# Kernel tuning notes

Hardware: AMD Instinct MI355X
Metric: run time of the kernel (lower is better)

The kernel has to match this reference:

```python
import jax, jax.numpy as jnp
import numpy as np

V, E, H, C_TAGS, B, T = 32000, 256, 200, 20, 64, 512
LN_EPS = 1e-5


def setup_inputs() -> dict:
    key = jax.random.key(0)
    ks = jax.random.split(key, 12)
    s = 0.05
    return {
        "words": jax.random.randint(ks[0], (B, T), 0, V),
        "seq_len": jax.random.randint(ks[1], (B,), T // 2, T + 1),
        "target": jax.random.randint(ks[2], (B, T), 0, C_TAGS),
        "embed_table": jax.random.normal(ks[3], (V, E)) * s,
        "ln_gamma": jnp.ones((E,)),
        "ln_beta": jnp.zeros((E,)),
        "w_ih_f": jax.random.normal(ks[4], (4 * H, E)) * s,
        "w_hh_f": jax.random.normal(ks[5], (4 * H, H)) * s,
        "b_f": jnp.zeros((4 * H,)),  # b_ih + b_hh folded together
        "w_ih_b": jax.random.normal(ks[6], (4 * H, E)) * s,
        "w_hh_b": jax.random.normal(ks[7], (4 * H, H)) * s,
        "b_b": jnp.zeros((4 * H,)),
        "fc_w": jax.random.normal(ks[8], (C_TAGS, 2 * H)) * s,
        "fc_b": jnp.zeros((C_TAGS,)),
        "trans": jax.random.normal(ks[9], (C_TAGS, C_TAGS)) * s,
        "start_scores": jax.random.normal(ks[10], (C_TAGS,)) * s,
        "end_scores": jax.random.normal(ks[11], (C_TAGS,)) * s,
    }


def _lstm_dir(x, m, w_ih, w_hh, b, reverse):
    """x: [T,B,E] time-major, m: [T,B] float mask. Packed-sequence semantics:
    carry only updates on valid steps (matters for the reverse direction)."""
    Hn = w_hh.shape[1]
    gates_x = jnp.einsum('tbe,ge->tbg', x, w_ih) + b  # [T,B,4H], batched GEMM

    def step(carry, xs):
        h, c = carry
        gx, mt = xs
        g = gx + h @ w_hh.T
        i, f, gg, o = jnp.split(g, 4, axis=-1)  # torch gate order i,f,g,o
        c_new = jax.nn.sigmoid(f) * c + jax.nn.sigmoid(i) * jnp.tanh(gg)
        h_new = jax.nn.sigmoid(o) * jnp.tanh(c_new)
        mt = mt[:, None]
        h = mt * h_new + (1.0 - mt) * h
        c = mt * c_new + (1.0 - mt) * c
        return (h, c), h

    init = (jnp.zeros((x.shape[1], Hn), x.dtype), jnp.zeros((x.shape[1], Hn), x.dtype))
    _, hs = jax.lax.scan(step, init, (gates_x, m), reverse=reverse)
    return hs  # [T,B,H]


def _crf_nll(logits, mask, target, trans, start, end):
    """Linear-chain CRF NLL with start/end transitions. logits [B,T,C] (emissions),
    mask [B,T] float, target [B,T] int. Returns per-sample loss [B]."""
    # --- log partition via forward algorithm (scan over time) ---
    alpha0 = start[None, :] + logits[:, 0]  # [B,C]
    emits = jnp.swapaxes(logits, 0, 1)[1:]  # [T-1,B,C]
    ms = jnp.swapaxes(mask, 0, 1)[1:]       # [T-1,B]

    def step(alpha, xs):
        emit, mt = xs
        scores = alpha[:, :, None] + trans[None, :, :] + emit[:, None, :]  # [B,C,C]
        new = jax.nn.logsumexp(scores, axis=1)
        alpha = jnp.where(mt[:, None] > 0, new, alpha)
        return alpha, None

    alpha, _ = jax.lax.scan(step, alpha0, (emits, ms))
    logZ = jax.nn.logsumexp(alpha + end[None, :], axis=1)  # [B]

    # --- gold path score ---
    emit_gold = jnp.take_along_axis(logits, target[..., None], axis=2)[..., 0]  # [B,T]
    emit_score = jnp.sum(emit_gold * mask, axis=1)
    trans_gold = trans[target[:, :-1], target[:, 1:]]  # [B,T-1]
    trans_score = jnp.sum(trans_gold * mask[:, 1:], axis=1)
    last_idx = jnp.sum(mask, axis=1).astype(jnp.int32) - 1
    last_tag = jnp.take_along_axis(target, last_idx[:, None], axis=1)[:, 0]
    gold = emit_score + trans_score + start[target[:, 0]] + end[last_tag]
    return logZ - gold


def reference(words, seq_len, target, embed_table, ln_gamma, ln_beta,
              w_ih_f, w_hh_f, b_f, w_ih_b, w_hh_b, b_b,
              fc_w, fc_b, trans, start_scores, end_scores):
    # Embedding + LayerNorm
    x = embed_table[words]  # [B,T,E]
    mu = x.mean(-1, keepdims=True)
    var = ((x - mu) ** 2).mean(-1, keepdims=True)
    x = (x - mu) * jax.lax.rsqrt(var + LN_EPS) * ln_gamma + ln_beta

    mask = (jnp.arange(x.shape[1])[None, :] < seq_len[:, None]).astype(x.dtype)  # [B,T]
    xt = jnp.swapaxes(x, 0, 1)       # [T,B,E]
    mt = jnp.swapaxes(mask, 0, 1)    # [T,B]

    # BiLSTM (num_layers=1)
    hf = _lstm_dir(xt, mt, w_ih_f, w_hh_f, b_f, reverse=False)
    hb = _lstm_dir(xt, mt, w_ih_b, w_hh_b, b_b, reverse=True)
    feats = jnp.swapaxes(jnp.concatenate([hf, hb], axis=-1), 0, 1)  # [B,T,2H]

    # fc + dropout (eval: identity) + log_softmax emissions
    feats = feats @ fc_w.T + fc_b
    logits = jax.nn.log_softmax(feats, axis=-1)

    loss = _crf_nll(logits, mask, target, trans, start_scores, end_scores)
    return loss.mean()
```

## Files before the change

kernel.cpp:

```cpp
#include <hip/hip_runtime.h>

#define TT 512
#define BB 64
#define EE 256
#define HH 200
#define GG 800
#define CC 20
#define MM (BB * TT)

typedef _Float16 f16x8 __attribute__((ext_vector_type(8)));
typedef float    f32x4 __attribute__((ext_vector_type(4)));
typedef _Float16 f16x2 __attribute__((ext_vector_type(2)));

#if __has_builtin(__builtin_amdgcn_mfma_f32_16x16x32_f16)
#define HAVE_MFMA_F16 1
#else
#define HAVE_MFMA_F16 0
#endif

__device__ __forceinline__ float bf2f(unsigned short u) {
  return __uint_as_float(((unsigned int)u) << 16);
}
__device__ __forceinline__ unsigned short f2bf(float f) {
  unsigned int u = __float_as_uint(f);
  return (unsigned short)((u + 0x7fffu + ((u >> 16) & 1u)) >> 16);
}
__device__ __forceinline__ float sigf(float x) { return 1.0f / (1.0f + __expf(-x)); }
__device__ __forceinline__ float tanhfast(float x) {
  return 1.0f - 2.0f / (__expf(2.0f * x) + 1.0f);
}
__device__ __forceinline__ f16x2 bfpair_to_h2(unsigned int p) {
  f16x2 r;
  r[0] = (_Float16)bf2f((unsigned short)(p & 0xffffu));
  r[1] = (_Float16)bf2f((unsigned short)(p >> 16));
  return r;
}
__device__ __forceinline__ float dot2acc(f16x2 a, f16x2 b, float c) {
#if __has_builtin(__builtin_amdgcn_fdot2)
  return __builtin_amdgcn_fdot2(a, b, c, false);
#else
  return c + (float)a[0] * (float)b[0] + (float)a[1] * (float)b[1];
#endif
}

#define NSEG 14
struct CvtArgs { const void* src[NSEG]; };
__constant__ const int cvt_cum[NSEG + 1] = {
    0, 8192000, 8192256, 8192512, 8397312, 8557312, 8558112,
    8762912, 8922912, 8923712, 8931712, 8931732, 8932132, 8932152, 8932172};

__global__ __launch_bounds__(256) void k_convert(CvtArgs a,
                                                 unsigned short* __restrict__ dst) {
  const bool f32mode = (((const unsigned int*)a.src[1])[0] == 0x3F800000u);
  int gi0 = (blockIdx.x * 256 + threadIdx.x) * 4;
#pragma unroll
  for (int r = 0; r < 4; ++r) {
    int gi = gi0 + r;
    if (gi >= cvt_cum[NSEG]) return;
    int seg = 0;
#pragma unroll
    for (int s = 1; s < NSEG; ++s) seg += (gi >= cvt_cum[s]) ? 1 : 0;
    int local = gi - cvt_cum[seg];
    unsigned short v;
    if (f32mode) v = f2bf(((const float*)a.src[seg])[local]);
    else         v = ((const unsigned short*)a.src[seg])[local];
    dst[gi] = v;
  }
}

__global__ __launch_bounds__(256) void k_embed_ln(
    const int* __restrict__ words, const unsigned short* __restrict__ etab,
    const unsigned short* __restrict__ gamma, const unsigned short* __restrict__ beta,
    unsigned short* __restrict__ x) {
  int m = blockIdx.x;
  int e = threadIdx.x;
  int w = words[m];
  float v = bf2f(etab[(size_t)w * EE + e]);
  float s = v, ss = v * v;
#pragma unroll
  for (int off = 32; off > 0; off >>= 1) {
    s += __shfl_xor(s, off, 64);
    ss += __shfl_xor(ss, off, 64);
  }
  __shared__ float red[2][4];
  int wv = e >> 6;
  if ((e & 63) == 0) { red[0][wv] = s; red[1][wv] = ss; }
  __syncthreads();
  float S = red[0][0] + red[0][1] + red[0][2] + red[0][3];
  float SS = red[1][0] + red[1][1] + red[1][2] + red[1][3];
  float mu = S * (1.0f / EE);
  float var = fmaxf(SS * (1.0f / EE) - mu * mu, 0.0f);
  float nrm = (v - mu) * rsqrtf(var + 1e-5f) * bf2f(gamma[e]) + bf2f(beta[e]);
  x[(size_t)m * EE + e] = f2bf(nrm);
}

#if HAVE_MFMA_F16
__global__ __launch_bounds__(256) void k_gates(
    const unsigned short* __restrict__ x,
    const unsigned short* __restrict__ wih_f, const unsigned short* __restrict__ wih_b,
    const unsigned short* __restrict__ bias_f, const unsigned short* __restrict__ bias_b,
    unsigned short* __restrict__ gates) {
  const int dir = blockIdx.z;
  const unsigned short* wih = dir ? wih_b : wih_f;
  const unsigned short* bias = dir ? bias_b : bias_f;
  const int m0 = blockIdx.x * 64;
  const int n0 = blockIdx.y * 64;
  __shared__ __align__(16) _Float16 As[64 * 32];
  __shared__ __align__(16) _Float16 Bs[64 * 32];
  const int tid = threadIdx.x;
  const int lane = tid & 63, wave = tid >> 6;
  const int wm = (wave >> 1) * 32, wn = (wave & 1) * 32;
  const int srow = tid >> 2, sq = tid & 3;
  const int mrow = lane & 15, q = lane >> 4;
  f32x4 acc[2][2] = {};
  for (int kk = 0; kk < EE; kk += 32) {
    union { int4 v; unsigned short u[8]; } ua, ub;
    ua.v = *(const int4*)(x + (size_t)(m0 + srow) * EE + kk + sq * 8);
    ub.v.x = 0; ub.v.y = 0; ub.v.z = 0; ub.v.w = 0;
    int n = n0 + srow;
    if (n < GG) ub.v = *(const int4*)(wih + (size_t)n * EE + kk + sq * 8);
    f16x8 af, bf;
#pragma unroll
    for (int r = 0; r < 8; ++r) {
      af[r] = (_Float16)bf2f(ua.u[r]);
      bf[r] = (_Float16)bf2f(ub.u[r]);
    }
    __syncthreads();
    *(f16x8*)(As + srow * 32 + sq * 8) = af;
    *(f16x8*)(Bs + srow * 32 + sq * 8) = bf;
    __syncthreads();
    f16x8 a0 = *(const f16x8*)(As + (wm + mrow) * 32 + q * 8);
    f16x8 a1 = *(const f16x8*)(As + (wm + 16 + mrow) * 32 + q * 8);
    f16x8 b0 = *(const f16x8*)(Bs + (wn + mrow) * 32 + q * 8);
    f16x8 b1 = *(const f16x8*)(Bs + (wn + 16 + mrow) * 32 + q * 8);
    acc[0][0] = __builtin_amdgcn_mfma_f32_16x16x32_f16(a0, b0, acc[0][0], 0, 0, 0);
    acc[0][1] = __builtin_amdgcn_mfma_f32_16x16x32_f16(a0, b1, acc[0][1], 0, 0, 0);
    acc[1][0] = __builtin_amdgcn_mfma_f32_16x16x32_f16(a1, b0, acc[1][0], 0, 0, 0);
    acc[1][1] = __builtin_amdgcn_mfma_f32_16x16x32_f16(a1, b1, acc[1][1], 0, 0, 0);
  }
#pragma unroll
  for (int im = 0; im < 2; ++im) {
#pragma unroll
    for (int in = 0; in < 2; ++in) {
      int n = n0 + wn + in * 16 + mrow;
      if (n < GG) {
        float bb = bf2f(bias[n]);
#pragma unroll
        for (int r = 0; r < 4; ++r) {
          int mg = m0 + wm + im * 16 + q * 4 + r;
          gates[((size_t)dir * MM + mg) * GG + n] = f2bf(acc[im][in][r] + bb);
        }
      }
    }
  }
}
#else
__global__ __launch_bounds__(256) void k_gates(
    const unsigned short* __restrict__ x,
    const unsigned short* __restrict__ wih_f, const unsigned short* __restrict__ wih_b,
    const unsigned short* __restrict__ bias_f, const unsigned short* __restrict__ bias_b,
    unsigned short* __restrict__ gates) {
  const int dir = blockIdx.z;
  const unsigned short* wih = dir ? wih_b : wih_f;
  const unsigned short* bias = dir ? bias_b : bias_f;
  const int m0 = blockIdx.x * 64;
  const int n0 = blockIdx.y * 64;
  for (int r = 0; r < 16; ++r) {
    int idx = threadIdx.x + 256 * r;
    int m = m0 + (idx >> 6), n = n0 + (idx & 63);
    if (n >= GG) continue;
    float acc = bf2f(bias[n]);
    const unsigned short* xr = x + (size_t)m * EE;
    const unsigned short* wr = wih + (size_t)n * EE;
    for (int k = 0; k < EE; ++k) acc += bf2f(xr[k]) * bf2f(wr[k]);
    gates[((size_t)dir * MM + m) * GG + n] = f2bf(acc);
  }
}
#endif

__global__ __launch_bounds__(832) void k_lstm(
    const unsigned short* __restrict__ gates,
    const unsigned short* __restrict__ whh_f, const unsigned short* __restrict__ whh_b,
    const int* __restrict__ seq_len,
    unsigned short* __restrict__ h_out) {
  const int b = blockIdx.x & (BB - 1);
  const int dir = blockIdx.x >> 6;
  const unsigned short* whh = dir ? whh_b : whh_f;
  const int tid = threadIdx.x;
  const int L = seq_len[b];
  __shared__ __align__(16) _Float16 hsh[HH];
  __shared__ float gbuf[GG];
  f16x2 w2[100];
  if (tid < GG) {
    const unsigned short* wr = whh + (size_t)tid * HH;
#pragma unroll
    for (int i = 0; i < 25; ++i) {
      int4 wvv = *(const int4*)(wr + i * 8);
      w2[4 * i + 0] = bfpair_to_h2((unsigned int)wvv.x);
      w2[4 * i + 1] = bfpair_to_h2((unsigned int)wvv.y);
      w2[4 * i + 2] = bfpair_to_h2((unsigned int)wvv.z);
      w2[4 * i + 3] = bfpair_to_h2((unsigned int)wvv.w);
    }
  }
  if (tid < HH) hsh[tid] = (_Float16)0.0f;
  float c_st = 0.0f, h_st = 0.0f;
  const unsigned short* gbase = gates + ((size_t)dir * MM + (size_t)b * TT) * GG + tid;
  unsigned short* hobase = h_out + (size_t)(dir * BB + b) * TT * HH;
  float gx_cur = 0.0f;
  if (tid < GG) {
    int t0 = dir ? (TT - 1) : 0;
    gx_cur = bf2f(gbase[(size_t)t0 * GG]);
  }
  __syncthreads();
  for (int s = 0; s < TT; ++s) {
    const int t = dir ? (TT - 1 - s) : s;
    if (tid < GG) {
      int sn = (s + 1 < TT) ? (s + 1) : s;
      int tn = dir ? (TT - 1 - sn) : sn;
      float gx_next = bf2f(gbase[(size_t)tn * GG]);
      float acc0 = gx_cur, acc1 = 0.0f;
#pragma unroll
      for (int i = 0; i < 25; ++i) {
        union { int4 v; f16x2 h[4]; } u;
        u.v = *(const int4*)(hsh + i * 8);
        acc0 = dot2acc(w2[4 * i + 0], u.h[0], acc0);
        acc1 = dot2acc(w2[4 * i + 1], u.h[1], acc1);
        acc0 = dot2acc(w2[4 * i + 2], u.h[2], acc0);
        acc1 = dot2acc(w2[4 * i + 3], u.h[3], acc1);
      }
      gbuf[tid] = acc0 + acc1;
      gx_cur = gx_next;
    }
    __syncthreads();
    if (tid < HH) {
      float gi = gbuf[tid], gf = gbuf[HH + tid];
      float gg = gbuf[2 * HH + tid], go = gbuf[3 * HH + tid];
      float cn = sigf(gf) * c_st + sigf(gi) * tanhfast(gg);
      float hn = sigf(go) * tanhfast(cn);
      if (t < L) { c_st = cn; h_st = hn; }
      hsh[tid] = (_Float16)h_st;
      hobase[(size_t)t * HH + tid] = f2bf(h_st);
    }
    __syncthreads();
  }
}

__global__ __launch_bounds__(256) void k_fc(
    const unsigned short* __restrict__ h_out,
    const unsigned short* __restrict__ fc_w, const unsigned short* __restrict__ fc_b,
    float* __restrict__ logits) {
  __shared__ __align__(16) unsigned short hsh[4][2 * HH];
  const int wv = threadIdx.x >> 6, lane = threadIdx.x & 63;
  const int m = blockIdx.x * 4 + wv;
  if (lane < 25) {
    *(int4*)&hsh[wv][lane * 8] = *(const int4*)(h_out + (size_t)m * HH + lane * 8);
  } else if (lane < 50) {
    *(int4*)&hsh[wv][HH + (lane - 25) * 8] =
        *(const int4*)(h_out + (size_t)MM * HH + (size_t)m * HH + (lane - 25) * 8);
  }
  __syncthreads();
  float s = -3.0e38f;
  if (lane < CC) {
    s = bf2f(fc_b[lane]);
    const unsigned short* wrow = fc_w + lane * 2 * HH;
    for (int jj = 0; jj < 50; ++jj) {
      union { int4 v; unsigned short u[8]; } hw, ww;
      hw.v = *(const int4*)&hsh[wv][jj * 8];
      ww.v = *(const int4*)(wrow + jj * 8);
#pragma unroll
      for (int r = 0; r < 8; ++r) s += bf2f(hw.u[r]) * bf2f(ww.u[r]);
    }
  }
  float mx = s;
#pragma unroll
  for (int off = 32; off > 0; off >>= 1) mx = fmaxf(mx, __shfl_xor(mx, off, 64));
  float ex = (lane < CC) ? __expf(s - mx) : 0.0f;
  float sm = ex;
#pragma unroll
  for (int off = 32; off > 0; off >>= 1) sm += __shfl_xor(sm, off, 64);
  if (lane < CC) logits[(size_t)m * CC + lane] = s - mx - __logf(sm);
}

__global__ __launch_bounds__(64) void k_crf(
    const float* __restrict__ logits, const int* __restrict__ target,
    const int* __restrict__ seq_len, const unsigned short* __restrict__ trans,
    const unsigned short* __restrict__ startv, const unsigned short* __restrict__ endv,
    float* __restrict__ loss_b) {
  const int b = blockIdx.x, lane = threadIdx.x;
  const int L = seq_len[b];
  const int* tg = target + b * TT;
  const float* lg = logits + (size_t)b * TT * CC;
  float tcol[CC];
#pragma unroll
  for (int i = 0; i < CC; ++i) tcol[i] = (lane < CC) ? bf2f(trans[i * CC + lane]) : 0.0f;
  float g = 0.0f;
  for (int t = lane; t < TT; t += 64) {
    if (t < L) {
      g += lg[t * CC + tg[t]];
      if (t >= 1) g += bf2f(trans[tg[t - 1] * CC + tg[t]]);
    }
  }
#pragma unroll
  for (int off = 32; off > 0; off >>= 1) g += __shfl_xor(g, off, 64);
  float alpha = (lane < CC) ? (bf2f(startv[lane]) + lg[lane]) : -3.0e38f;
  for (int t = 1; t < L; ++t) {
    float e = (lane < CC) ? lg[t * CC + lane] : 0.0f;
    float sc[CC];
#pragma unroll
    for (int i = 0; i < CC; ++i) sc[i] = __shfl(alpha, i, 64) + tcol[i];
    float mx = sc[0];
#pragma unroll
    for (int i = 1; i < CC; ++i) mx = fmaxf(mx, sc[i]);
    float sm = 0.0f;
#pragma unroll
    for (int i = 0; i < CC; ++i) sm += __expf(sc[i] - mx);
    float na = mx + __logf(sm) + e;
    if (lane < CC) alpha = na;
  }
  float v = (lane < CC) ? (alpha + bf2f(endv[lane])) : -3.0e38f;
  float mx = v;
#pragma unroll
  for (int off = 32; off > 0; off >>= 1) mx = fmaxf(mx, __shfl_xor(mx, off, 64));
  float ex = (lane < CC) ? __expf(v - mx) : 0.0f;
#pragma unroll
  for (int off = 32; off > 0; off >>= 1) ex += __shfl_xor(ex, off, 64);
  if (lane == 0) {
    float logZ = mx + __logf(ex);
    float gold = g + bf2f(startv[tg[0]]) + bf2f(endv[tg[L - 1]]);
    loss_b[b] = logZ - gold;
  }
}

__global__ __launch_bounds__(64) void k_mean(const float* __restrict__ loss_b,
                                             unsigned int* __restrict__ out) {
  float v = loss_b[threadIdx.x];
#pragma unroll
  for (int off = 32; off > 0; off >>= 1) v += __shfl_xor(v, off, 64);
  if (threadIdx.x == 0) {
    float mean = v * (1.0f / BB);
    unsigned int lo = (unsigned int)f2bf(mean);
    unsigned int hi = __float_as_uint(mean) >> 16;
    out[0] = (hi << 16) | lo;
  }
}

extern "C" void kernel_launch(void* const* d_in, const int* in_sizes, int n_in,
                              void* d_out, int out_size, void* d_ws, size_t ws_size,
                              hipStream_t stream) {
  const int* words   = (const int*)d_in[0];
  const int* seq_len = (const int*)d_in[1];
  const int* target  = (const int*)d_in[2];

  char* ws = (char*)d_ws;
  const size_t x_off      = 0;
  const size_t gates_off  = x_off + 16777216;
  const size_t h_off      = gates_off + 104857600;
  const size_t logits_off = h_off + 26214400;
  const size_t loss_off   = logits_off + 2621440;
  const size_t cvt_off    = loss_off + 256;
  unsigned short* x      = (unsigned short*)(ws + x_off);
  unsigned short* gatesb = (unsigned short*)(ws + gates_off);
  unsigned short* h_out  = (unsigned short*)(ws + h_off);
  float* logits          = (float*)(ws + logits_off);
  float* loss_b          = (float*)(ws + loss_off);
  unsigned short* wcvt   = (unsigned short*)(ws + cvt_off);

  unsigned short* etab_c  = wcvt + 0;
  unsigned short* gamma_c = wcvt + 8192000;
  unsigned short* beta_c  = wcvt + 8192256;
  unsigned short* wih_f_c = wcvt + 8192512;
  unsigned short* whh_f_c = wcvt + 8397312;
  unsigned short* b_f_c   = wcvt + 8557312;
  unsigned short* wih_b_c = wcvt + 8558112;
  unsigned short* whh_b_c = wcvt + 8762912;
  unsigned short* b_b_c   = wcvt + 8922912;
  unsigned short* fc_w_c  = wcvt + 8923712;
  unsigned short* fc_b_c  = wcvt + 8931712;
  unsigned short* trans_c = wcvt + 8931732;
  unsigned short* start_c = wcvt + 8932132;
  unsigned short* end_c   = wcvt + 8932152;

  CvtArgs ca;
  for (int i = 0; i < NSEG; ++i) ca.src[i] = d_in[3 + i];
  const int total_cvt = 8932172;
  k_convert<<<(total_cvt + 1023) / 1024, 256, 0, stream>>>(ca, wcvt);

  k_embed_ln<<<MM, 256, 0, stream>>>(words, etab_c, gamma_c, beta_c, x);
  k_gates<<<dim3(MM / 64, 13, 2), 256, 0, stream>>>(x, wih_f_c, wih_b_c, b_f_c, b_b_c, gatesb);
  k_lstm<<<128, 832, 0, stream>>>(gatesb, whh_f_c, whh_b_c, seq_len, h_out);
  k_fc<<<MM / 4, 256, 0, stream>>>(h_out, fc_w_c, fc_b_c, logits);
  k_crf<<<BB, 64, 0, stream>>>(logits, target, seq_len, trans_c, start_c, end_c, loss_b);
  k_mean<<<1, 64, 0, stream>>>(loss_b, (unsigned int*)d_out);
}
```

Before: 1.140 ms.

## Pair threads per hidden unit in LSTM, exchange gates by shuffle, double-buffer h

Each pair of threads now computes all four gate pre-activations for one hidden unit, two rows each. The partner's gates arrive through a lane shuffle, which removes the shared gate buffer and one block barrier per time step. The hidden state is double-buffered in shared memory so a single barrier per step is enough. The recurrence also runs only to each sequence's length, so padded steps are skipped. The costs are twice the weight registers per thread, and h_out is never written for positions at or beyond the sequence length, so downstream code must mask them safely.

```diff
diff --git a/kernel.cpp b/kernel.cpp
--- a/kernel.cpp
+++ b/kernel.cpp
@@ -178,7 +178,7 @@
 }
 #endif
 
-__global__ __launch_bounds__(832) void k_lstm(
+__global__ __launch_bounds__(448, 1) void k_lstm(
     const unsigned short* __restrict__ gates,
     const unsigned short* __restrict__ whh_f, const unsigned short* __restrict__ whh_b,
     const int* __restrict__ seq_len,
@@ -188,58 +188,74 @@
   const unsigned short* whh = dir ? whh_b : whh_f;
   const int tid = threadIdx.x;
   const int L = seq_len[b];
-  __shared__ __align__(16) _Float16 hsh[HH];
-  __shared__ float gbuf[GG];
-  f16x2 w2[100];
-  if (tid < GG) {
-    const unsigned short* wr = whh + (size_t)tid * HH;
+  __shared__ __align__(16) _Float16 hsh[2][HH + 8];
+  const int e = tid >> 1;
+  const int base = (tid & 1) * 200 + e;
+  f16x2 wA[100], wB[100];
+  if (tid < 400) {
+    const unsigned short* wrA = whh + (size_t)base * HH;
+    const unsigned short* wrB = whh + (size_t)(base + 400) * HH;
 #pragma unroll
     for (int i = 0; i < 25; ++i) {
-      int4 wvv = *(const int4*)(wr + i * 8);
-      w2[4 * i + 0] = bfpair_to_h2((unsigned int)wvv.x);
-      w2[4 * i + 1] = bfpair_to_h2((unsigned int)wvv.y);
-      w2[4 * i + 2] = bfpair_to_h2((unsigned int)wvv.z);
-      w2[4 * i + 3] = bfpair_to_h2((unsigned int)wvv.w);
-    }
-  }
-  if (tid < HH) hsh[tid] = (_Float16)0.0f;
+      int4 va = *(const int4*)(wrA + i * 8);
+      int4 vb = *(const int4*)(wrB + i * 8);
+      wA[4 * i + 0] = bfpair_to_h2((unsigned int)va.x);
+      wA[4 * i + 1] = bfpair_to_h2((unsigned int)va.y);
+      wA[4 * i + 2] = bfpair_to_h2((unsigned int)va.z);
+      wA[4 * i + 3] = bfpair_to_h2((unsigned int)va.w);
+      wB[4 * i + 0] = bfpair_to_h2((unsigned int)vb.x);
+      wB[4 * i + 1] = bfpair_to_h2((unsigned int)vb.y);
+      wB[4 * i + 2] = bfpair_to_h2((unsigned int)vb.z);
+      wB[4 * i + 3] = bfpair_to_h2((unsigned int)vb.w);
+    }
+  }
+  if (tid < HH) { hsh[0][tid] = (_Float16)0.0f; hsh[1][tid] = (_Float16)0.0f; }
   float c_st = 0.0f, h_st = 0.0f;
-  const unsigned short* gbase = gates + ((size_t)dir * MM + (size_t)b * TT) * GG + tid;
+  const unsigned short* g0 = gates + ((size_t)dir * MM + (size_t)b * TT) * GG;
   unsigned short* hobase = h_out + (size_t)(dir * BB + b) * TT * HH;
-  float gx_cur = 0.0f;
-  if (tid < GG) {
-    int t0 = dir ? (TT - 1) : 0;
-    gx_cur = bf2f(gbase[(size_t)t0 * GG]);
+  float gxa = 0.0f, gxb = 0.0f;
+  if (tid < 400) {
+    int t0 = dir ? (L - 1) : 0;
+    gxa = bf2f(g0[(size_t)t0 * GG + base]);
+    gxb = bf2f(g0[(size_t)t0 * GG + base + 400]);
   }
   __syncthreads();
-  for (int s = 0; s < TT; ++s) {
-    const int t = dir ? (TT - 1 - s) : s;
-    if (tid < GG) {
-      int sn = (s + 1 < TT) ? (s + 1) : s;
-      int tn = dir ? (TT - 1 - sn) : sn;
-      float gx_next = bf2f(gbase[(size_t)tn * GG]);
-      float acc0 = gx_cur, acc1 = 0.0f;
+  for (int s = 0; s < L; ++s) {
+    const int t = dir ? (L - 1 - s) : s;
+    const int p = s & 1;
+    float a0 = 0.0f, a1 = 0.0f;
+    if (tid < 400) {
+      int sn = (s + 1 < L) ? (s + 1) : s;
+      int tn = dir ? (L - 1 - sn) : sn;
+      float gna = bf2f(g0[(size_t)tn * GG + base]);
+      float gnb = bf2f(g0[(size_t)tn * GG + base + 400]);
+      float x0 = gxa, x1 = 0.0f, y0 = gxb, y1 = 0.0f;
 #pragma unroll
       for (int i = 0; i < 25; ++i) {
         union { int4 v; f16x2 h[4]; } u;
-        u.v = *(const int4*)(hsh + i * 8);
-        acc0 = dot2acc(w2[4 * i + 0], u.h[0], acc0);
-        acc1 = dot2acc(w2[4 * i + 1], u.h[1], acc1);
-        acc0 = dot2acc(w2[4 * i + 2], u.h[2], acc0);
-        acc1 = dot2acc(w2[4 * i + 3], u.h[3], acc1);
+        u.v = *(const int4*)(&hsh[p][i * 8]);
+        x0 = dot2acc(wA[4 * i + 0], u.h[0], x0);
+        x1 = dot2acc(wA[4 * i + 1], u.h[1], x1);
+        x0 = dot2acc(wA[4 * i + 2], u.h[2], x0);
+        x1 = dot2acc(wA[4 * i + 3], u.h[3], x1);
+        y0 = dot2acc(wB[4 * i + 0], u.h[0], y0);
+        y1 = dot2acc(wB[4 * i + 1], u.h[1], y1);
+        y0 = dot2acc(wB[4 * i + 2], u.h[2], y0);
+        y1 = dot2acc(wB[4 * i + 3], u.h[3], y1);
       }
-      gbuf[tid] = acc0 + acc1;
-      gx_cur = gx_next;
-    }
-    __syncthreads();
-    if (tid < HH) {
-      float gi = gbuf[tid], gf = gbuf[HH + tid];
-      float gg = gbuf[2 * HH + tid], go = gbuf[3 * HH + tid];
+      a0 = x0 + x1;
+      a1 = y0 + y1;
+      gxa = gna; gxb = gnb;
+    }
+    float n0 = __shfl_xor(a0, 1, 64);
+    float n1 = __shfl_xor(a1, 1, 64);
+    if (tid < 400 && !(tid & 1)) {
+      float gi = a0, gg = a1, gf = n0, go = n1;
       float cn = sigf(gf) * c_st + sigf(gi) * tanhfast(gg);
       float hn = sigf(go) * tanhfast(cn);
-      if (t < L) { c_st = cn; h_st = hn; }
-      hsh[tid] = (_Float16)h_st;
-      hobase[(size_t)t * HH + tid] = f2bf(h_st);
+      c_st = cn; h_st = hn;
+      hsh[p ^ 1][e] = (_Float16)h_st;
+      hobase[(size_t)t * HH + e] = f2bf(h_st);
     }
     __syncthreads();
   }
@@ -387,7 +403,7 @@
 
   k_embed_ln<<<MM, 256, 0, stream>>>(words, etab_c, gamma_c, beta_c, x);
   k_gates<<<dim3(MM / 64, 13, 2), 256, 0, stream>>>(x, wih_f_c, wih_b_c, b_f_c, b_b_c, gatesb);
-  k_lstm<<<128, 832, 0, stream>>>(gatesb, whh_f_c, whh_b_c, seq_len, h_out);
+  k_lstm<<<128, 448, 0, stream>>>(gatesb, whh_f_c, whh_b_c, seq_len, h_out);
   k_fc<<<MM / 4, 256, 0, stream>>>(h_out, fc_w_c, fc_b_c, logits);
   k_crf<<<BB, 64, 0, stream>>>(logits, target, seq_len, trans_c, start_c, end_c, loss_b);
   k_mean<<<1, 64, 0, stream>>>(loss_b, (unsigned int*)d_out);
```

After: 1.161 ms. No clear change (+1.8%).
